# Kernel tuning notes

Hardware: AMD Instinct MI355X
Metric: run time of the kernel (lower is better)

Reference implementation:

```python
import jax, jax.numpy as jnp
import numpy as np

HIDDEN = 1024
NUM_HEADS = 16
HEAD_SIZE = HIDDEN // NUM_HEADS
B, S = 2, 2048


def setup_inputs() -> dict:
    key = jax.random.key(0)
    k_x, k_wqkv, k_bqkv, k_wo, k_bo = jax.random.split(key, 5)
    x = jax.random.normal(k_x, (B, S, HIDDEN), dtype=jnp.float32)
    # Dense kernels, fan-in scaled like lecun_normal init
    Wqkv = jax.random.normal(k_wqkv, (HIDDEN, 3 * HIDDEN), dtype=jnp.float32) / np.sqrt(HIDDEN)
    bqkv = jnp.zeros((3 * HIDDEN,), dtype=jnp.float32)
    Wo = jax.random.normal(k_wo, (HIDDEN, HIDDEN), dtype=jnp.float32) / np.sqrt(HIDDEN)
    bo = jnp.zeros((HIDDEN,), dtype=jnp.float32)
    return {"x": x, "Wqkv": Wqkv, "bqkv": bqkv, "Wo": Wo, "bo": bo}


def reference(x, Wqkv, bqkv, Wo, bo):
    b, s, h = x.shape
    qkv = jnp.einsum('bsh,hf->bsf', x, Wqkv) + bqkv          # [b, s, 3*h]
    qkv = qkv.reshape(b, s, 3, NUM_HEADS, HEAD_SIZE)
    q, k, v = qkv[:, :, 0], qkv[:, :, 1], qkv[:, :, 2]        # [b, s, nh, hd]
    scale = 1.0 / np.sqrt(HEAD_SIZE)
    scores = jnp.einsum('bqhd,bkhd->bhqk', q, k) * scale      # [b, nh, s, s]
    weights = jax.nn.softmax(scores, axis=-1)
    attn = jnp.einsum('bhqk,bkhd->bqhd', weights, v)          # [b, s, nh, hd]
    attn = attn.reshape(b, s, h)
    return jnp.einsum('bsh,hf->bsf', attn, Wo) + bo
```

## Files before the change

### kernel.cpp

```cpp
#include <hip/hip_runtime.h>
#include <hip/hip_bf16.h>

#define HIDDEN 1024
#define NH 16
#define BATCH 2
#define SEQ 2048

typedef __attribute__((ext_vector_type(8))) short bf16x8;
typedef __attribute__((ext_vector_type(4))) float f32x4;

__device__ __forceinline__ ushort f2bf(float f) {
    __hip_bfloat16 h = __float2bfloat16(f);
    return *reinterpret_cast<ushort*>(&h);
}
__device__ __forceinline__ float bf2f(ushort u) {
    __hip_bfloat16 h;
    *reinterpret_cast<ushort*>(&h) = u;
    return __bfloat162float(h);
}

__device__ __forceinline__ void async_copy16(const ushort* g, ushort* l) {
    __builtin_amdgcn_global_load_lds((const __attribute__((address_space(1))) void*)g,
                                     (__attribute__((address_space(3))) void*)l,
                                     16, 0, 0);
}

__global__ void prep_kernel(const float* __restrict__ x,
                            const float* __restrict__ Wqkv,
                            const float* __restrict__ Wo,
                            ushort* __restrict__ xb,
                            ushort* __restrict__ Wt,
                            ushort* __restrict__ WoT_hi,
                            ushort* __restrict__ WoT_lo)
{
    __shared__ float t[32][33];
    const int bid = blockIdx.x;
    const int tid = threadIdx.x;

    if (bid < 4096) {
        int i = (bid * 256 + tid) * 4;
        float4 v = *(const float4*)(x + i);
        ushort4 w;
        w.x = f2bf(v.x); w.y = f2bf(v.y); w.z = f2bf(v.z); w.w = f2bf(v.w);
        *(ushort4*)(xb + i) = w;
        return;
    }
    const int r = tid >> 3;
    const int c = (tid & 7) * 4;
    if (bid < 7168) {
        int tt = bid - 4096;
        int k0 = (tt & 31) * 32;
        int n0 = (tt >> 5) * 32;
        const int N = 3 * HIDDEN, K = HIDDEN;
        float4 v = *(const float4*)(Wqkv + (size_t)(k0 + r) * N + n0 + c);
        t[r][c] = v.x; t[r][c + 1] = v.y; t[r][c + 2] = v.z; t[r][c + 3] = v.w;
        __syncthreads();
        ushort4 w;
        w.x = f2bf(t[c + 0][r]); w.y = f2bf(t[c + 1][r]);
        w.z = f2bf(t[c + 2][r]); w.w = f2bf(t[c + 3][r]);
        *(ushort4*)(Wt + (size_t)(n0 + r) * K + k0 + c) = w;
    } else {
        int tt = bid - 7168;
        int k0 = (tt & 31) * 32;
        int n0 = (tt >> 5) * 32;
        const int N = HIDDEN, K = HIDDEN;
        float4 v = *(const float4*)(Wo + (size_t)(k0 + r) * N + n0 + c);
        t[r][c] = v.x; t[r][c + 1] = v.y; t[r][c + 2] = v.z; t[r][c + 3] = v.w;
        __syncthreads();
        ushort4 whi, wlo;
        float vv;
        vv = t[c + 0][r]; whi.x = f2bf(vv); wlo.x = f2bf(vv - bf2f(whi.x));
        vv = t[c + 1][r]; whi.y = f2bf(vv); wlo.y = f2bf(vv - bf2f(whi.y));
        vv = t[c + 2][r]; whi.z = f2bf(vv); wlo.z = f2bf(vv - bf2f(whi.z));
        vv = t[c + 3][r]; whi.w = f2bf(vv); wlo.w = f2bf(vv - bf2f(whi.w));
        *(ushort4*)(WoT_hi + (size_t)(n0 + r) * K + k0 + c) = whi;
        *(ushort4*)(WoT_lo + (size_t)(n0 + r) * K + k0 + c) = wlo;
    }
}

__global__ void transpose_v_kernel(const ushort* __restrict__ qkvb,
                                   ushort* __restrict__ vtg)
{
    __shared__ ushort T[64][72];
    int blk = blockIdx.x;
    int st = blk & 31;
    int h  = (blk >> 5) & 15;
    int b  = blk >> 9;
    int s0 = st * 64;

    int s  = threadIdx.x >> 2;
    int c0 = (threadIdx.x & 3) * 2;
    const ushort* src = qkvb + ((size_t)(b * SEQ + s0 + s)) * 3072 + 2048 + h * 64;
    *(uint4*)&T[s][c0 * 8]     = *(const uint4*)(src + c0 * 8);
    *(uint4*)&T[s][c0 * 8 + 8] = *(const uint4*)(src + c0 * 8 + 8);
    __syncthreads();

    int d = threadIdx.x >> 2;
    ushort* dst = vtg + ((size_t)((b * NH + h) * 64 + d)) * SEQ + s0;
    #pragma unroll
    for (int cc = 0; cc < 2; cc++) {
        int c2 = (threadIdx.x & 3) * 2 + cc;
        ushort tmp[8];
        #pragma unroll
        for (int j = 0; j < 8; j++) {
            int sp = c2 * 8 + j;
            int key = (sp & 3) * 16 + (sp >> 2);
            tmp[j] = T[key][d];
        }
        *(uint4*)(dst + c2 * 8) = *(const uint4*)tmp;
    }
}

__global__ __launch_bounds__(256, 3)
void gemm_mfma_bf16_kernel(const ushort* __restrict__ A,
                           const ushort* __restrict__ Bt,
                           const float* __restrict__ bias,
                           ushort* __restrict__ C, int N,
                           int qscale_cols)
{
    constexpr int K = 1024;
    __shared__ ushort As[128 * 64];
    __shared__ ushort Bs[128 * 64];

    const int tid  = threadIdx.x;
    const int wave = tid >> 6;
    const int lane = tid & 63;
    const int l16  = lane & 15;
    const int quad = lane >> 4;
    const int wm = wave & 1, wn = wave >> 1;

    const int bm = blockIdx.y * 128;
    const int bn = blockIdx.x * 128;

    const int srow = lane >> 3;
    const int lblk = (lane & 7) ^ srow;
    const ushort* Ag = A  + (size_t)(bm + wave * 32 + srow) * K + lblk * 8;
    const ushort* Bg = Bt + (size_t)(bn + wave * 32 + srow) * K + lblk * 8;
    ushort* Asl = As + wave * 32 * 64;
    ushort* Bsl = Bs + wave * 32 * 64;

    f32x4 acc[4][4];
    #pragma unroll
    for (int i = 0; i < 4; i++)
        #pragma unroll
        for (int j = 0; j < 4; j++) acc[i][j] = (f32x4){0.f, 0.f, 0.f, 0.f};

    for (int k0 = 0; k0 < K; k0 += 64) {
        __syncthreads();
        #pragma unroll
        for (int t = 0; t < 4; t++) {
            async_copy16(Ag + (size_t)t * 8 * K + k0, Asl + t * 8 * 64);
            async_copy16(Bg + (size_t)t * 8 * K + k0, Bsl + t * 8 * 64);
        }
        __syncthreads();

        #pragma unroll
        for (int s = 0; s < 2; s++) {
            bf16x8 af[4], bfr[4];
            #pragma unroll
            for (int i = 0; i < 4; i++) {
                int m = wm * 64 + i * 16 + l16;
                int n = wn * 64 + i * 16 + l16;
                af[i]  = *(const bf16x8*)&As[m * 64 + (((s * 4 + quad) ^ (m & 7)) << 3)];
                bfr[i] = *(const bf16x8*)&Bs[n * 64 + (((s * 4 + quad) ^ (n & 7)) << 3)];
            }
            #pragma unroll
            for (int i = 0; i < 4; i++)
                #pragma unroll
                for (int j = 0; j < 4; j++)
                    acc[i][j] = __builtin_amdgcn_mfma_f32_16x16x32_bf16(af[i], bfr[j], acc[i][j], 0, 0, 0);
        }
    }

    #pragma unroll
    for (int j = 0; j < 4; j++) {
        int col = bn + wn * 64 + j * 16 + l16;
        float bv = bias[col];
        float s = (col < qscale_cols) ? 0.125f : 1.0f;
        #pragma unroll
        for (int i = 0; i < 4; i++) {
            int row0 = bm + wm * 64 + i * 16 + quad * 4;
            #pragma unroll
            for (int r = 0; r < 4; r++)
                C[(size_t)(row0 + r) * N + col] = f2bf((acc[i][j][r] + bv) * s);
        }
    }
}

__global__ __launch_bounds__(256, 2)
void gemm3_split_kernel(const ushort* __restrict__ Ahi,
                        const ushort* __restrict__ Alo,
                        const ushort* __restrict__ Bthi,
                        const ushort* __restrict__ Btlo,
                        const float* __restrict__ bias,
                        float* __restrict__ C)
{
    constexpr int K = 1024, N = 1024;
    __shared__ ushort AsHi[128 * 64];
    __shared__ ushort AsLo[128 * 64];
    __shared__ ushort BsHi[64 * 64];
    __shared__ ushort BsLo[64 * 64];

    const int tid  = threadIdx.x;
    const int wave = tid >> 6;
    const int lane = tid & 63;
    const int l16  = lane & 15;
    const int quad = lane >> 4;
    const int wm = wave & 1, wn = wave >> 1;

    const int bm = blockIdx.y * 128;
    const int bn = blockIdx.x * 64;

    const int srow = lane >> 3;
    const int lblk = (lane & 7) ^ srow;
    const size_t aoff = (size_t)(bm + wave * 32 + srow) * K + lblk * 8;
    const size_t boff = (size_t)(bn + wave * 16 + srow) * K + lblk * 8;
    const ushort* AgHi = Ahi + aoff;
    const ushort* AgLo = Alo + aoff;
    const ushort* BgHi = Bthi + boff;
    const ushort* BgLo = Btlo + boff;
    ushort* AslHi = AsHi + wave * 32 * 64;
    ushort* AslLo = AsLo + wave * 32 * 64;
    ushort* BslHi = BsHi + wave * 16 * 64;
    ushort* BslLo = BsLo + wave * 16 * 64;

    f32x4 acc[4][2];
    #pragma unroll
    for (int i = 0; i < 4; i++)
        #pragma unroll
        for (int j = 0; j < 2; j++) acc[i][j] = (f32x4){0.f, 0.f, 0.f, 0.f};

    for (int k0 = 0; k0 < K; k0 += 64) {
        __syncthreads();
        #pragma unroll
        for (int t = 0; t < 4; t++) {
            async_copy16(AgHi + (size_t)t * 8 * K + k0, AslHi + t * 8 * 64);
            async_copy16(AgLo + (size_t)t * 8 * K + k0, AslLo + t * 8 * 64);
        }
        #pragma unroll
        for (int t = 0; t < 2; t++) {
            async_copy16(BgHi + (size_t)t * 8 * K + k0, BslHi + t * 8 * 64);
            async_copy16(BgLo + (size_t)t * 8 * K + k0, BslLo + t * 8 * 64);
        }
        __syncthreads();

        #pragma unroll
        for (int s = 0; s < 2; s++) {
            bf16x8 ah[4], al[4], bh[2], bl[2];
            #pragma unroll
            for (int i = 0; i < 4; i++) {
                int m = wm * 64 + i * 16 + l16;
                int idx = m * 64 + (((s * 4 + quad) ^ (m & 7)) << 3);
                ah[i] = *(const bf16x8*)&AsHi[idx];
                al[i] = *(const bf16x8*)&AsLo[idx];
            }
            #pragma unroll
            for (int j = 0; j < 2; j++) {
                int n = wn * 32 + j * 16 + l16;
                int idx = n * 64 + (((s * 4 + quad) ^ (n & 7)) << 3);
                bh[j] = *(const bf16x8*)&BsHi[idx];
                bl[j] = *(const bf16x8*)&BsLo[idx];
            }
            #pragma unroll
            for (int i = 0; i < 4; i++)
                #pragma unroll
                for (int j = 0; j < 2; j++) {
                    acc[i][j] = __builtin_amdgcn_mfma_f32_16x16x32_bf16(ah[i], bh[j], acc[i][j], 0, 0, 0);
                    acc[i][j] = __builtin_amdgcn_mfma_f32_16x16x32_bf16(ah[i], bl[j], acc[i][j], 0, 0, 0);
                    acc[i][j] = __builtin_amdgcn_mfma_f32_16x16x32_bf16(al[i], bh[j], acc[i][j], 0, 0, 0);
                }
        }
    }

    #pragma unroll
    for (int j = 0; j < 2; j++) {
        int col = bn + wn * 32 + j * 16 + l16;
        float bv = bias[col];
        #pragma unroll
        for (int i = 0; i < 4; i++) {
            int row0 = bm + wm * 64 + i * 16 + quad * 4;
            #pragma unroll
            for (int r = 0; r < 4; r++)
                C[(size_t)(row0 + r) * N + col] = acc[i][j][r] + bv;
        }
    }
}

__global__ __launch_bounds__(512, 4)
void attn_mfma_kernel(const ushort* __restrict__ qkvb,
                      const ushort* __restrict__ vtg,
                      int use_vtg,
                      ushort* __restrict__ attn_hi,
                      ushort* __restrict__ attn_lo)
{
    __shared__ __align__(16) ushort smem[34816];

    const int tid   = threadIdx.x;
    const int wave  = tid >> 6;
    const int wavel = wave & 3;
    const int kh    = wave >> 2;
    const int lane  = tid & 63;
    const int l16   = lane & 15;
    const int quad  = lane >> 4;

    const int qb = blockIdx.x & 15;
    const int bh = blockIdx.x >> 4;
    const int h  = bh & (NH - 1);
    const int b  = bh >> 4;

    const int qbase = qb * 128;
    const int hoff  = h * 64;

    ushort* KsH = smem + kh * 4096;
    ushort* VsH = smem + 8192 + kh * 4096;
    ushort* Psw = smem + 16384 + wave * 2304;

    bf16x8 a_q[2][2];
    #pragma unroll
    for (int mg = 0; mg < 2; mg++) {
        int qrow = b * SEQ + qbase + wavel * 32 + mg * 16 + l16;
        const ushort* qp = qkvb + (size_t)qrow * 3072 + hoff + quad * 8;
        a_q[mg][0] = *(const bf16x8*)qp;
        a_q[mg][1] = *(const bf16x8*)(qp + 32);
    }

    f32x4 o[2][4];
    f32x4 lacc[2];
    #pragma unroll
    for (int mg = 0; mg < 2; mg++) {
        lacc[mg] = (f32x4){0.f, 0.f, 0.f, 0.f};
        #pragma unroll
        for (int nt = 0; nt < 4; nt++) o[mg][nt] = (f32x4){0.f, 0.f, 0.f, 0.f};
    }

    bf16x8 b_ones;
    #pragma unroll
    for (int j = 0; j < 8; j++) b_ones[j] = (short)0x3f80;

    const ushort* kvb    = qkvb + (size_t)b * SEQ * 3072;
    const ushort* vtg_bh = vtg + (size_t)((b * NH + h) * 64) * SEQ;

    const int srow8 = lane >> 3;
    const int gblk  = ((lane & 7) ^ srow8) << 3;
    const ushort* kg = kvb + (size_t)(kh * 1024 + wavel * 16 + srow8) * 3072 + 1024 + hoff + gblk;
    const ushort* vg = vtg_bh + (size_t)(wavel * 16 + srow8) * SEQ + kh * 1024 + gblk;

    for (int t = 0; t < 16; t++) {
        const int k0 = t * 64;
        __syncthreads();
        if (use_vtg) {
            #pragma unroll
            for (int c = 0; c < 2; c++) {
                async_copy16(kg + (size_t)(k0 + c * 8) * 3072, KsH + (wavel * 16 + c * 8) * 64);
                async_copy16(vg + (size_t)(c * 8) * SEQ + k0,  VsH + (wavel * 16 + c * 8) * 64);
            }
        } else {
            const int tl = tid & 255;
            #pragma unroll
            for (int i = 0; i < 2; i++) {
                int key = (tl >> 3) + 32 * i;
                int blk = tl & 7;
                const ushort* ksrc = kvb + (size_t)(kh * 1024 + k0 + key) * 3072 + 1024 + hoff + blk * 8;
                uint4 kv = *(const uint4*)ksrc;
                *(uint4*)&KsH[key * 64 + ((blk ^ (key & 7)) << 3)] = kv;
                uint4 vv = *(const uint4*)(ksrc + 1024);
                const ushort* vp = (const ushort*)&vv;
                int pk_ = (key & 15) * 4 + (key >> 4);
                #pragma unroll
                for (int j = 0; j < 8; j++) {
                    int d = blk * 8 + j;
                    VsH[d * 64 + (((pk_ >> 3) ^ (d & 7)) << 3) + (pk_ & 7)] = vp[j];
                }
            }
        }
        __syncthreads();

        f32x4 sc[2][4];
        #pragma unroll
        for (int nt = 0; nt < 4; nt++) {
            int key = nt * 16 + l16;
            bf16x8 bk0 = *(const bf16x8*)&KsH[key * 64 + ((quad ^ (key & 7)) << 3)];
            bf16x8 bk1 = *(const bf16x8*)&KsH[key * 64 + (((4 + quad) ^ (key & 7)) << 3)];
            #pragma unroll
            for (int mg = 0; mg < 2; mg++) {
                f32x4 a = (f32x4){0.f, 0.f, 0.f, 0.f};
                a = __builtin_amdgcn_mfma_f32_16x16x32_bf16(a_q[mg][0], bk0, a, 0, 0, 0);
                a = __builtin_amdgcn_mfma_f32_16x16x32_bf16(a_q[mg][1], bk1, a, 0, 0, 0);
                sc[mg][nt] = a;
            }
        }

        #pragma unroll
        for (int mg = 0; mg < 2; mg++) {
            #pragma unroll
            for (int r = 0; r < 4; r++) {
                int q = mg * 16 + quad * 4 + r;
                uint2 pk2;
                pk2.x = (uint)f2bf(__expf(sc[mg][0][r])) |
                        ((uint)f2bf(__expf(sc[mg][1][r])) << 16);
                pk2.y = (uint)f2bf(__expf(sc[mg][2][r])) |
                        ((uint)f2bf(__expf(sc[mg][3][r])) << 16);
                *(uint2*)&Psw[q * 72 + l16 * 4] = pk2;
            }
        }

        asm volatile("s_waitcnt lgkmcnt(0)" ::: "memory");
        bf16x8 a_p[2][2];
        #pragma unroll
        for (int mg = 0; mg < 2; mg++) {
            a_p[mg][0] = *(const bf16x8*)&Psw[(mg * 16 + l16) * 72 + quad * 8];
            a_p[mg][1] = *(const bf16x8*)&Psw[(mg * 16 + l16) * 72 + 32 + quad * 8];
        }

        #pragma unroll
        for (int nt = 0; nt < 4; nt++) {
            int d = nt * 16 + l16;
            bf16x8 bv0 = *(const bf16x8*)&VsH[d * 64 + ((quad ^ (d & 7)) << 3)];
            bf16x8 bv1 = *(const bf16x8*)&VsH[d * 64 + (((4 + quad) ^ (d & 7)) << 3)];
            #pragma unroll
            for (int mg = 0; mg < 2; mg++) {
                o[mg][nt] = __builtin_amdgcn_mfma_f32_16x16x32_bf16(a_p[mg][0], bv0, o[mg][nt], 0, 0, 0);
                o[mg][nt] = __builtin_amdgcn_mfma_f32_16x16x32_bf16(a_p[mg][1], bv1, o[mg][nt], 0, 0, 0);
            }
        }
        #pragma unroll
        for (int mg = 0; mg < 2; mg++) {
            lacc[mg] = __builtin_amdgcn_mfma_f32_16x16x32_bf16(a_p[mg][0], b_ones, lacc[mg], 0, 0, 0);
            lacc[mg] = __builtin_amdgcn_mfma_f32_16x16x32_bf16(a_p[mg][1], b_ones, lacc[mg], 0, 0, 0);
        }
    }

    __syncthreads();
    float* osc = (float*)smem;
    float* lsc = (float*)(smem + 16384);
    const int fo = wavel * 2048 + quad * 64 + l16 * 4;
    const int fl = wavel * 512 + quad * 64 + l16 * 4;
    if (kh == 1) {
        #pragma unroll
        for (int mg = 0; mg < 2; mg++) {
            #pragma unroll
            for (int nt = 0; nt < 4; nt++)
                *(f32x4*)&osc[fo + (mg * 4 + nt) * 256] = o[mg][nt];
            *(f32x4*)&lsc[fl + mg * 256] = lacc[mg];
        }
    }
    __syncthreads();
    if (kh == 0) {
        #pragma unroll
        for (int mg = 0; mg < 2; mg++) {
            #pragma unroll
            for (int nt = 0; nt < 4; nt++)
                o[mg][nt] += *(const f32x4*)&osc[fo + (mg * 4 + nt) * 256];
            lacc[mg] += *(const f32x4*)&lsc[fl + mg * 256];
        }
        #pragma unroll
        for (int mg = 0; mg < 2; mg++) {
            #pragma unroll
            for (int r = 0; r < 4; r++) {
                float inv = 1.f / lacc[mg][r];
                int row = b * SEQ + qbase + wavel * 32 + mg * 16 + quad * 4 + r;
                size_t base = (size_t)row * HIDDEN + hoff + l16;
                #pragma unroll
                for (int nt = 0; nt < 4; nt++) {
                    float val = o[mg][nt][r] * inv;
                    ushort hi = f2bf(val);
                    ushort lo = f2bf(val - bf2f(hi));
                    attn_hi[base + nt * 16] = hi;
                    attn_lo[base + nt * 16] = lo;
                }
            }
        }
    }
}

extern "C" void kernel_launch(void* const* d_in, const int* in_sizes, int n_in,
                              void* d_out, int out_size, void* d_ws, size_t ws_size,
                              hipStream_t stream) {
    const float* x    = (const float*)d_in[0];
    const float* Wqkv = (const float*)d_in[1];
    const float* bqkv = (const float*)d_in[2];
    const float* Wo   = (const float*)d_in[3];
    const float* bo   = (const float*)d_in[4];
    float* out = (float*)d_out;

    const int M = BATCH * SEQ;
    const size_t MB = 1024 * 1024;

    char* ws = (char*)d_ws;
    ushort* qkvb    = (ushort*)ws;
    ushort* attn_hi = (ushort*)(ws + 24 * MB);
    ushort* attn_lo = (ushort*)(ws + 32 * MB);
    ushort* xb      = (ushort*)(ws + 24 * MB);
    ushort* Wt      = (ushort*)(ws + 32 * MB);
    ushort* WoT_hi  = (ushort*)(ws + 40 * MB);
    ushort* WoT_lo  = (ushort*)(ws + 42 * MB);
    ushort* vtg     = (ushort*)(ws + 44 * MB);
    const int use_vtg = (ws_size >= 52 * MB) ? 1 : 0;

    prep_kernel<<<8192, 256, 0, stream>>>(x, Wqkv, Wo, xb, Wt, WoT_hi, WoT_lo);

    {
        dim3 grid((3 * HIDDEN) / 128, M / 128);
        gemm_mfma_bf16_kernel<<<grid, 256, 0, stream>>>(xb, Wt, bqkv, qkvb,
                                                        3 * HIDDEN, HIDDEN);
    }

    if (use_vtg) {
        transpose_v_kernel<<<BATCH * NH * (SEQ / 64), 256, 0, stream>>>(qkvb, vtg);
    }

    attn_mfma_kernel<<<BATCH * NH * (SEQ / 128), 512, 0, stream>>>(qkvb, vtg, use_vtg,
                                                                   attn_hi, attn_lo);

    {
        dim3 grid(HIDDEN / 64, M / 128);
        gemm3_split_kernel<<<grid, 256, 0, stream>>>(attn_hi, attn_lo,
                                                     WoT_hi, WoT_lo, bo, out);
    }
}
```

Before: 199.6 us.

## Add LDS-free direct-load attention kernel with exp2 and truncating bf16 pack

```diff
diff --git a/kernel.cpp b/kernel.cpp
--- a/kernel.cpp
+++ b/kernel.cpp
@@ -17,6 +17,16 @@
     __hip_bfloat16 h;
     *reinterpret_cast<ushort*>(&h) = u;
     return __bfloat162float(h);
+}
+__device__ __forceinline__ float fexp2(float x) {
+#if __has_builtin(__builtin_amdgcn_exp2f)
+    return __builtin_amdgcn_exp2f(x);
+#else
+    return exp2f(x);
+#endif
+}
+__device__ __forceinline__ uint pack_bf_trunc(float a, float b) {
+    return __builtin_amdgcn_perm(__float_as_uint(b), __float_as_uint(a), 0x07060302u);
 }
 
 __device__ __forceinline__ void async_copy16(const ushort* g, ushort* l) {
@@ -116,7 +126,7 @@
                            const ushort* __restrict__ Bt,
                            const float* __restrict__ bias,
                            ushort* __restrict__ C, int N,
-                           int qscale_cols)
+                           int qscale_cols, float qscale)
 {
     constexpr int K = 1024;
     __shared__ ushort As[128 * 64];
@@ -176,7 +186,7 @@
     for (int j = 0; j < 4; j++) {
         int col = bn + wn * 64 + j * 16 + l16;
         float bv = bias[col];
-        float s = (col < qscale_cols) ? 0.125f : 1.0f;
+        float s = (col < qscale_cols) ? qscale : 1.0f;
         #pragma unroll
         for (int i = 0; i < 4; i++) {
             int row0 = bm + wm * 64 + i * 16 + quad * 4;
@@ -286,12 +296,196 @@
     }
 }
 
+__global__ __launch_bounds__(256)
+void attn_mfma_direct_kernel(const ushort* __restrict__ qkvb,
+                             const ushort* __restrict__ vtg,
+                             ushort* __restrict__ attn_hi,
+                             ushort* __restrict__ attn_lo)
+{
+    __shared__ __align__(16) ushort smem[4 * 2304 + 64];
+
+    const int tid  = threadIdx.x;
+    const int kh   = tid >> 6;
+    const int lane = tid & 63;
+    const int l16  = lane & 15;
+    const int quad = lane >> 4;
+
+    const int qb = blockIdx.x & 63;
+    const int bh = blockIdx.x >> 6;
+    const int h  = bh & (NH - 1);
+    const int b  = bh >> 4;
+
+    const int qbase = qb * 32;
+    const int hoff  = h * 64;
+
+    ushort* Psw = smem + kh * 2304;
+
+    bf16x8 a_q[2][2];
+    #pragma unroll
+    for (int mg = 0; mg < 2; mg++) {
+        int qrow = b * SEQ + qbase + mg * 16 + l16;
+        const ushort* qp = qkvb + (size_t)qrow * 3072 + hoff + quad * 8;
+        a_q[mg][0] = *(const bf16x8*)qp;
+        a_q[mg][1] = *(const bf16x8*)(qp + 32);
+    }
+
+    f32x4 o[2][4];
+    f32x4 lacc[2];
+    #pragma unroll
+    for (int mg = 0; mg < 2; mg++) {
+        lacc[mg] = (f32x4){0.f, 0.f, 0.f, 0.f};
+        #pragma unroll
+        for (int nt = 0; nt < 4; nt++) o[mg][nt] = (f32x4){0.f, 0.f, 0.f, 0.f};
+    }
+
+    bf16x8 b_ones;
+    #pragma unroll
+    for (int j = 0; j < 8; j++) b_ones[j] = (short)0x3f80;
+
+    const ushort* kvb    = qkvb + (size_t)b * SEQ * 3072;
+    const ushort* vtg_bh = vtg + (size_t)((b * NH + h) * 64) * SEQ;
+    const ushort* kp[4];
+    const ushort* vp[4];
+    #pragma unroll
+    for (int nt = 0; nt < 4; nt++) {
+        kp[nt] = kvb + (size_t)(kh * 512 + nt * 16 + l16) * 3072 + 1024 + hoff + quad * 8;
+        vp[nt] = vtg_bh + (size_t)(nt * 16 + l16) * SEQ + kh * 512 + quad * 8;
+    }
+
+    for (int t = 0; t < 8; t++) {
+        bf16x8 kf[4][2], vf[4][2];
+        #pragma unroll
+        for (int nt = 0; nt < 4; nt++) {
+            kf[nt][0] = *(const bf16x8*)kp[nt];
+            kf[nt][1] = *(const bf16x8*)(kp[nt] + 32);
+        }
+        #pragma unroll
+        for (int nt = 0; nt < 4; nt++) {
+            vf[nt][0] = *(const bf16x8*)vp[nt];
+            vf[nt][1] = *(const bf16x8*)(vp[nt] + 32);
+        }
+
+        f32x4 sc[2][4];
+        #pragma unroll
+        for (int nt = 0; nt < 4; nt++) {
+            #pragma unroll
+            for (int mg = 0; mg < 2; mg++) {
+                f32x4 a = (f32x4){0.f, 0.f, 0.f, 0.f};
+                a = __builtin_amdgcn_mfma_f32_16x16x32_bf16(a_q[mg][0], kf[nt][0], a, 0, 0, 0);
+                a = __builtin_amdgcn_mfma_f32_16x16x32_bf16(a_q[mg][1], kf[nt][1], a, 0, 0, 0);
+                sc[mg][nt] = a;
+            }
+        }
+
+        #pragma unroll
+        for (int mg = 0; mg < 2; mg++) {
+            #pragma unroll
+            for (int r = 0; r < 4; r++) {
+                int q = mg * 16 + quad * 4 + r;
+                uint2 pk2;
+                pk2.x = pack_bf_trunc(fexp2(sc[mg][0][r]), fexp2(sc[mg][1][r]));
+                pk2.y = pack_bf_trunc(fexp2(sc[mg][2][r]), fexp2(sc[mg][3][r]));
+                *(uint2*)&Psw[q * 72 + l16 * 4] = pk2;
+            }
+        }
+
+        asm volatile("s_waitcnt lgkmcnt(0)" ::: "memory");
+        bf16x8 a_p[2][2];
+        #pragma unroll
+        for (int mg = 0; mg < 2; mg++) {
+            a_p[mg][0] = *(const bf16x8*)&Psw[(mg * 16 + l16) * 72 + quad * 8];
+            a_p[mg][1] = *(const bf16x8*)&Psw[(mg * 16 + l16) * 72 + 32 + quad * 8];
+        }
+
+        #pragma unroll
+        for (int nt = 0; nt < 4; nt++) {
+            #pragma unroll
+            for (int mg = 0; mg < 2; mg++) {
+                o[mg][nt] = __builtin_amdgcn_mfma_f32_16x16x32_bf16(a_p[mg][0], vf[nt][0], o[mg][nt], 0, 0, 0);
+                o[mg][nt] = __builtin_amdgcn_mfma_f32_16x16x32_bf16(a_p[mg][1], vf[nt][1], o[mg][nt], 0, 0, 0);
+            }
+        }
+        #pragma unroll
+        for (int mg = 0; mg < 2; mg++) {
+            lacc[mg] = __builtin_amdgcn_mfma_f32_16x16x32_bf16(a_p[mg][0], b_ones, lacc[mg], 0, 0, 0);
+            lacc[mg] = __builtin_amdgcn_mfma_f32_16x16x32_bf16(a_p[mg][1], b_ones, lacc[mg], 0, 0, 0);
+        }
+
+        #pragma unroll
+        for (int nt = 0; nt < 4; nt++) {
+            kp[nt] += (size_t)64 * 3072;
+            vp[nt] += 64;
+        }
+    }
+
+    float* osc = (float*)smem;
+    float* lsc = (float*)smem + 4096;
+    #define O_SLOT(rgn, mg, nt) (&osc[(rgn) * 2048 + (((mg) * 4 + (nt)) * 4 + quad) * 64 + l16 * 4])
+    #define L_SLOT(rgn, mg)     (&lsc[(rgn) * 32 + ((mg) * 4 + quad) * 4])
+
+    __syncthreads();
+    if (kh == 1 || kh == 3) {
+        int rgn = kh >> 1;
+        #pragma unroll
+        for (int mg = 0; mg < 2; mg++) {
+            #pragma unroll
+            for (int nt = 0; nt < 4; nt++) *(f32x4*)O_SLOT(rgn, mg, nt) = o[mg][nt];
+            if (l16 == 0) *(f32x4*)L_SLOT(rgn, mg) = lacc[mg];
+        }
+    }
+    __syncthreads();
+    if (kh == 0 || kh == 2) {
+        int rgn = kh >> 1;
+        #pragma unroll
+        for (int mg = 0; mg < 2; mg++) {
+            #pragma unroll
+            for (int nt = 0; nt < 4; nt++) o[mg][nt] += *(const f32x4*)O_SLOT(rgn, mg, nt);
+            lacc[mg] += *(const f32x4*)L_SLOT(rgn, mg);
+        }
+    }
+    __syncthreads();
+    if (kh == 2) {
+        #pragma unroll
+        for (int mg = 0; mg < 2; mg++) {
+            #pragma unroll
+            for (int nt = 0; nt < 4; nt++) *(f32x4*)O_SLOT(0, mg, nt) = o[mg][nt];
+            if (l16 == 0) *(f32x4*)L_SLOT(0, mg) = lacc[mg];
+        }
+    }
+    __syncthreads();
+    if (kh == 0) {
+        #pragma unroll
+        for (int mg = 0; mg < 2; mg++) {
+            #pragma unroll
+            for (int nt = 0; nt < 4; nt++) o[mg][nt] += *(const f32x4*)O_SLOT(0, mg, nt);
+            lacc[mg] += *(const f32x4*)L_SLOT(0, mg);
+        }
+        #pragma unroll
+        for (int mg = 0; mg < 2; mg++) {
+            #pragma unroll
+            for (int r = 0; r < 4; r++) {
+                float inv = 1.f / lacc[mg][r];
+                int row = b * SEQ + qbase + mg * 16 + quad * 4 + r;
+                size_t base = (size_t)row * HIDDEN + hoff + l16;
+                #pragma unroll
+                for (int nt = 0; nt < 4; nt++) {
+                    float val = o[mg][nt][r] * inv;
+                    ushort hi = f2bf(val);
+                    ushort lo = f2bf(val - bf2f(hi));
+                    attn_hi[base + nt * 16] = hi;
+                    attn_lo[base + nt * 16] = lo;
+                }
+            }
+        }
+    }
+    #undef O_SLOT
+    #undef L_SLOT
+}
+
 __global__ __launch_bounds__(512, 4)
-void attn_mfma_kernel(const ushort* __restrict__ qkvb,
-                      const ushort* __restrict__ vtg,
-                      int use_vtg,
-                      ushort* __restrict__ attn_hi,
-                      ushort* __restrict__ attn_lo)
+void attn_mfma_fb_kernel(const ushort* __restrict__ qkvb,
+                         ushort* __restrict__ attn_hi,
+                         ushort* __restrict__ attn_lo)
 {
     __shared__ __align__(16) ushort smem[34816];
 
@@ -337,24 +531,12 @@
     #pragma unroll
     for (int j = 0; j < 8; j++) b_ones[j] = (short)0x3f80;
 
-    const ushort* kvb    = qkvb + (size_t)b * SEQ * 3072;
-    const ushort* vtg_bh = vtg + (size_t)((b * NH + h) * 64) * SEQ;
-
-    const int srow8 = lane >> 3;
-    const int gblk  = ((lane & 7) ^ srow8) << 3;
-    const ushort* kg = kvb + (size_t)(kh * 1024 + wavel * 16 + srow8) * 3072 + 1024 + hoff + gblk;
-    const ushort* vg = vtg_bh + (size_t)(wavel * 16 + srow8) * SEQ + kh * 1024 + gblk;
+    const ushort* kvb = qkvb + (size_t)b * SEQ * 3072;
 
     for (int t = 0; t < 16; t++) {
         const int k0 = t * 64;
         __syncthreads();
-        if (use_vtg) {
-            #pragma unroll
-            for (int c = 0; c < 2; c++) {
-                async_copy16(kg + (size_t)(k0 + c * 8) * 3072, KsH + (wavel * 16 + c * 8) * 64);
-                async_copy16(vg + (size_t)(c * 8) * SEQ + k0,  VsH + (wavel * 16 + c * 8) * 64);
-            }
-        } else {
+        {
             const int tl = tid & 255;
             #pragma unroll
             for (int i = 0; i < 2; i++) {
@@ -364,12 +546,12 @@
                 uint4 kv = *(const uint4*)ksrc;
                 *(uint4*)&KsH[key * 64 + ((blk ^ (key & 7)) << 3)] = kv;
                 uint4 vv = *(const uint4*)(ksrc + 1024);
-                const ushort* vp = (const ushort*)&vv;
+                const ushort* vpp = (const ushort*)&vv;
                 int pk_ = (key & 15) * 4 + (key >> 4);
                 #pragma unroll
                 for (int j = 0; j < 8; j++) {
                     int d = blk * 8 + j;
-                    VsH[d * 64 + (((pk_ >> 3) ^ (d & 7)) << 3) + (pk_ & 7)] = vp[j];
+                    VsH[d * 64 + (((pk_ >> 3) ^ (d & 7)) << 3) + (pk_ & 7)] = vpp[j];
                 }
             }
         }
@@ -396,10 +578,8 @@
             for (int r = 0; r < 4; r++) {
                 int q = mg * 16 + quad * 4 + r;
                 uint2 pk2;
-                pk2.x = (uint)f2bf(__expf(sc[mg][0][r])) |
-                        ((uint)f2bf(__expf(sc[mg][1][r])) << 16);
-                pk2.y = (uint)f2bf(__expf(sc[mg][2][r])) |
-                        ((uint)f2bf(__expf(sc[mg][3][r])) << 16);
+                pk2.x = pack_bf_trunc(fexp2(sc[mg][0][r]), fexp2(sc[mg][1][r]));
+                pk2.y = pack_bf_trunc(fexp2(sc[mg][2][r]), fexp2(sc[mg][3][r]));
                 *(uint2*)&Psw[q * 72 + l16 * 4] = pk2;
             }
         }
@@ -497,20 +677,24 @@
     ushort* vtg     = (ushort*)(ws + 44 * MB);
     const int use_vtg = (ws_size >= 52 * MB) ? 1 : 0;
 
+    const float qscale = 0.125f * 1.44269504088896f;
+
     prep_kernel<<<8192, 256, 0, stream>>>(x, Wqkv, Wo, xb, Wt, WoT_hi, WoT_lo);
 
     {
         dim3 grid((3 * HIDDEN) / 128, M / 128);
         gemm_mfma_bf16_kernel<<<grid, 256, 0, stream>>>(xb, Wt, bqkv, qkvb,
-                                                        3 * HIDDEN, HIDDEN);
+                                                        3 * HIDDEN, HIDDEN, qscale);
     }
 
     if (use_vtg) {
         transpose_v_kernel<<<BATCH * NH * (SEQ / 64), 256, 0, stream>>>(qkvb, vtg);
-    }
-
-    attn_mfma_kernel<<<BATCH * NH * (SEQ / 128), 512, 0, stream>>>(qkvb, vtg, use_vtg,
-                                                                   attn_hi, attn_lo);
+        attn_mfma_direct_kernel<<<BATCH * NH * (SEQ / 32), 256, 0, stream>>>(
+            qkvb, vtg, attn_hi, attn_lo);
+    } else {
+        attn_mfma_fb_kernel<<<BATCH * NH * (SEQ / 128), 512, 0, stream>>>(
+            qkvb, attn_hi, attn_lo);
+    }
 
     {
         dim3 grid(HIDDEN / 64, M / 128);
```

New measurement: 267.1 us. 33.9% more time.
